# Kernel optimization log

Measured on AMD Instinct MI355X. Metric: run time of the kernel, lower is better.

The kernel has to match this reference:

```python
import jax, jax.numpy as jnp
import numpy as np

GAMMA = 0.9  # decay (init kwarg)


def setup_inputs() -> dict:
    key = jax.random.key(0)
    k0, k1, k2, k3 = jax.random.split(key, 4)
    B, T, D = 16, 2048, 256
    x = jax.random.normal(k0, (B, T, D), jnp.float32)
    scale = 1.0 / np.sqrt(D)
    Wq = jax.random.normal(k1, (D, D), jnp.float32) * scale
    Wk = jax.random.normal(k2, (D, D), jnp.float32) * scale
    Wv = jax.random.normal(k3, (D, D), jnp.float32) * scale
    return {"x": x, "Wq": Wq, "Wk": Wk, "Wv": Wv}


def reference(x, Wq, Wk, Wv):
    # x: [B, T, D]
    B, T, D = x.shape
    Q = x @ Wq  # [B, T, D]
    K = x @ Wk
    V = x @ Wv

    # Sequential retention recurrence over the [D, D] state:
    #   s[t] = gamma * s[t-1] + K[:, t, :]^T @ V[:, t, :]   (sums over batch, as in source)
    Kt = jnp.swapaxes(K, 0, 1)  # [T, B, D]
    Vt = jnp.swapaxes(V, 0, 1)  # [T, B, D]

    def step(s, kv):
        k_t, v_t = kv  # each [B, D]
        s = GAMMA * s + k_t.T @ v_t  # [D, D]
        return s, s.sum(-1)  # emit row-sum [D]

    # Loop runs t = 1 .. T-1 in the source (s starts at 0); s[0] := s[1].
    init = jnp.zeros((D, D), x.dtype)
    _, rows = jax.lax.scan(step, init, (Kt[1:], Vt[1:]))  # rows: [T-1, D]
    S = jnp.concatenate([rows[:1], rows], axis=0)  # [T, D]

    # Faithful to tf.reshape(S, [-1, seq_len]) then tf.transpose: a reshape-scramble,
    # NOT a plain transpose of S.
    S2 = S.reshape(D, T).T  # [T, D]
    return S2[None, :, :] * Q  # broadcast over batch -> [B, T, D]
```

## Files before the change

### kernel.cpp

```cpp
#include <hip/hip_runtime.h>
#include <math.h>


#define GAMMA_F 0.9f
#define T_LEN 2048
#define D_DIM 256
#define B_DIM 16

typedef __attribute__((ext_vector_type(8))) short bf16x8;
typedef __attribute__((ext_vector_type(16))) float f32x16;

__device__ inline ushort f2bf(float f) {
    union { float f; unsigned u; } v; v.f = f;
    unsigned r = (v.u + 0x7FFFu + ((v.u >> 16) & 1u)) >> 16;
    return (ushort)r;
}

__device__ __forceinline__ void gload_lds16(const void* g, void* l) {
    __builtin_amdgcn_global_load_lds(
        (const __attribute__((address_space(1))) unsigned int*)g,
        (__attribute__((address_space(3))) unsigned int*)l, 16, 0, 0);
}

__global__ __launch_bounds__(256) void k_prep(const float* __restrict__ Wq,
                                              const float* __restrict__ Wk,
                                              const float* __restrict__ Wv,
                                              ushort* __restrict__ WqT,
                                              ushort* __restrict__ WkT,
                                              float* __restrict__ wv_sum) {
    int bid = blockIdx.x;
    int tid = threadIdx.x;
    if (bid < 32) {
        __shared__ float tile[64][68];
        const float* W = (bid < 16) ? Wq : Wk;
        ushort* WT = (bid < 16) ? WqT : WkT;
        int b = bid & 15;
        int k0 = (b & 3) * 64;
        int n0 = (b >> 2) * 64;
        int r = tid >> 4;
        int c4 = (tid & 15) * 4;
#pragma unroll
        for (int i = 0; i < 4; ++i) {
            float4 v = *(const float4*)(W + (size_t)(k0 + r + 16 * i) * D_DIM + n0 + c4);
            *(float4*)&tile[r + 16 * i][c4] = v;
        }
        __syncthreads();
        int n = tid >> 2;
        int j0 = (tid & 3) * 16;
        ushort tmp[16];
#pragma unroll
        for (int i = 0; i < 16; ++i) tmp[i] = f2bf(tile[j0 + i][n]);
        ushort* dst = WT + (size_t)(n0 + n) * D_DIM + k0 + j0;
#pragma unroll
        for (int i = 0; i < 16; ++i) dst[i] = tmp[i];
    } else {
        int j = (bid - 32) * 64 + (tid >> 2);
        int q = tid & 3;
        const float4* row4 = (const float4*)(Wv + (size_t)j * D_DIM + q * 64);
        float s = 0.f;
#pragma unroll
        for (int i = 0; i < 16; ++i) {
            float4 v = row4[i];
            s += v.x + v.y + v.z + v.w;
        }
        s += __shfl_xor(s, 1, 64);
        s += __shfl_xor(s, 2, 64);
        if (q == 0) wv_sum[j] = s;
    }
}

__global__ __launch_bounds__(256) void k_y(const float* __restrict__ x,
                                           const float* __restrict__ wv_sum,
                                           ushort* __restrict__ ybf,
                                           ushort* __restrict__ xbf) {
    int t = blockIdx.x;
    int d = threadIdx.x;
    float wvd = wv_sum[d];
    float xr[B_DIM];
#pragma unroll
    for (int b = 0; b < B_DIM; ++b)
        xr[b] = x[((size_t)b * T_LEN + t) * D_DIM + d];

#pragma unroll
    for (int b = 0; b < B_DIM; ++b)
        xbf[((size_t)b * T_LEN + t) * D_DIM + d] = f2bf(xr[b]);

    __shared__ float red[B_DIM][4];
    int wave = d >> 6, lane = d & 63;
#pragma unroll
    for (int b = 0; b < B_DIM; ++b) {
        float p = xr[b] * wvd;
        for (int o = 32; o > 0; o >>= 1) p += __shfl_down(p, o, 64);
        if (lane == 0) red[b][wave] = p;
    }
    __syncthreads();
    float yv = 0.f;
#pragma unroll
    for (int b = 0; b < B_DIM; ++b) {
        float wb = red[b][0] + red[b][1] + red[b][2] + red[b][3];
        yv += wb * xr[b];
    }
    ybf[(size_t)t * D_DIM + d] = f2bf(yv);
}

__global__ __launch_bounds__(256) void k_gs(const ushort* __restrict__ ybf,
                                            const ushort* __restrict__ WkT,
                                            float* __restrict__ loc,
                                            float* __restrict__ carry) {
    __shared__ ushort As[32 * 64 * 8];
    __shared__ ushort Bs[32 * 64 * 8];
    float* Cs = (float*)As;
    int mt = blockIdx.x >> 2;
    int nt = blockIdx.x & 3;
    int tid = threadIdx.x, lane = tid & 63, w = tid >> 6;
    int wr = w >> 1, wc = w & 1, l31 = lane & 31, lh = lane >> 5;

#pragma unroll
    for (int i = 0; i < 8; ++i) {
        int slot = tid + 256 * i;
        int r = slot >> 5;
        int s2h = slot & 31;
        int rs = r ^ (s2h & 7);
        *(bf16x8*)&As[(s2h * 64 + rs) * 8] =
            *(const bf16x8*)&ybf[(size_t)(mt * 64 + r) * D_DIM + s2h * 8];
        *(bf16x8*)&Bs[(s2h * 64 + rs) * 8] =
            *(const bf16x8*)&WkT[(size_t)(nt * 64 + r) * D_DIM + s2h * 8];
    }
    __syncthreads();

    f32x16 acc;
#pragma unroll
    for (int e = 0; e < 16; ++e) acc[e] = 0.f;
#pragma unroll
    for (int s = 0; s < 16; ++s) {
        int s2h = s * 2 + lh;
        int ra = (wr * 32 + l31) ^ (s2h & 7);
        int rb = (wc * 32 + l31) ^ (s2h & 7);
        bf16x8 a = *(bf16x8*)&As[(s2h * 64 + ra) * 8];
        bf16x8 b = *(bf16x8*)&Bs[(s2h * 64 + rb) * 8];
        acc = __builtin_amdgcn_mfma_f32_32x32x16_bf16(a, b, acc, 0, 0, 0);
    }
    __syncthreads();

#pragma unroll
    for (int reg = 0; reg < 16; ++reg) {
        int rr = (reg & 3) + 8 * (reg >> 2) + 4 * lh;
        Cs[(wr * 32 + rr) * 64 + wc * 32 + l31] = acc[reg];
    }
    __syncthreads();

#pragma unroll
    for (int half = 0; half < 2; ++half) {
        int task = half * 256 + tid;
        int dl = task & 63;
        int cl = task >> 6;
        float a = 0.f;
#pragma unroll
        for (int j = 0; j < 8; ++j) {
            int tl = cl * 8 + j;
            int gt = mt * 64 + tl;
            float v = (gt == 0) ? 0.f : Cs[tl * 64 + dl];
            a = GAMMA_F * a + v;
            loc[(size_t)gt * D_DIM + nt * 64 + dl] = a;
        }
        carry[(size_t)(mt * 8 + cl) * D_DIM + nt * 64 + dl] = a;
    }
}

__global__ __launch_bounds__(256) void k_S2P(const float* __restrict__ loc,
                                             const float* __restrict__ carry,
                                             float* __restrict__ S2) {
    __shared__ float Ls[256][33];
    int o = blockIdx.x >> 3;
    int dseg = blockIdx.x & 7;
    int r = threadIdx.x;
    int dstart = dseg * 32;
    const float g8 = 0.43046721f;
    const float log2g = -0.15200309344504995f;
    float gp = exp2f((float)(o + 1) * log2g);

    float p = 0.f;
    int j0 = dstart - 32; if (j0 < 0) j0 = 0;
    for (int j = j0; j < dstart; ++j)
        p = p * g8 + carry[(size_t)j * D_DIM + r];

#pragma unroll
    for (int dd = 0; dd < 32; ++dd) {
        int d_ = dstart + dd;
        float Aval = loc[(size_t)(8 * d_ + o) * D_DIM + r] + gp * p;
        if (o == 0 && d_ == 0) Aval = loc[D_DIM + r];
        Ls[r][dd] = Aval;
        p = p * g8 + carry[(size_t)d_ * D_DIM + r];
    }
    __syncthreads();

    int rr = threadIdx.x >> 3;
    int cq = threadIdx.x & 7;
#pragma unroll
    for (int it = 0; it < 8; ++it) {
        int row = it * 32 + rr;
        float4 v;
        v.x = Ls[row][cq * 4 + 0];
        v.y = Ls[row][cq * 4 + 1];
        v.z = Ls[row][cq * 4 + 2];
        v.w = Ls[row][cq * 4 + 3];
        *(float4*)&S2[(size_t)((o << 8) + row) * D_DIM + dstart + cq * 4] = v;
    }
}

__global__ __launch_bounds__(256) void k_qgemm(const ushort* __restrict__ xbf,
                                               const ushort* __restrict__ WqT,
                                               const float* __restrict__ S2,
                                               float* __restrict__ out) {
    __shared__ ushort As[8 * 128 * 8];
    __shared__ ushort Bs[8 * 128 * 8];
    int bid = blockIdx.x;
    int mb = bid >> 1;
    int nb = bid & 1;
    int tid = threadIdx.x;
    int lane = tid & 63, w = tid >> 6;
    int wr = w >> 1, wc = w & 1;
    int l31 = lane & 31, lh = lane >> 5;

    f32x16 acc[2][2];
#pragma unroll
    for (int i = 0; i < 2; ++i)
#pragma unroll
        for (int j = 0; j < 2; ++j)
#pragma unroll
            for (int e = 0; e < 16; ++e) acc[i][j][e] = 0.f;

    const ushort* ab = xbf + (size_t)mb * 128 * D_DIM;
    const ushort* bb = WqT + (size_t)nb * 128 * D_DIM;

    for (int kb = 0; kb < 4; ++kb) {
#pragma unroll
        for (int i = 0; i < 4; ++i) {
            int slot = i * 256 + tid;
            int kk = slot >> 7;
            int row = slot & 127;
            int ldsbase = (i * 256 + w * 64) * 8;
            gload_lds16(ab + (size_t)row * D_DIM + kb * 64 + kk * 8, &As[ldsbase]);
            gload_lds16(bb + (size_t)row * D_DIM + kb * 64 + kk * 8, &Bs[ldsbase]);
        }
        __syncthreads();
#pragma unroll
        for (int s = 0; s < 4; ++s) {
            int c0 = (s * 2 + lh) * 128;
            bf16x8 a0 = *(bf16x8*)&As[(c0 + wr * 64 + l31) * 8];
            bf16x8 a1 = *(bf16x8*)&As[(c0 + wr * 64 + 32 + l31) * 8];
            bf16x8 b0 = *(bf16x8*)&Bs[(c0 + wc * 64 + l31) * 8];
            bf16x8 b1 = *(bf16x8*)&Bs[(c0 + wc * 64 + 32 + l31) * 8];
            acc[0][0] = __builtin_amdgcn_mfma_f32_32x32x16_bf16(a0, b0, acc[0][0], 0, 0, 0);
            acc[0][1] = __builtin_amdgcn_mfma_f32_32x32x16_bf16(a0, b1, acc[0][1], 0, 0, 0);
            acc[1][0] = __builtin_amdgcn_mfma_f32_32x32x16_bf16(a1, b0, acc[1][0], 0, 0, 0);
            acc[1][1] = __builtin_amdgcn_mfma_f32_32x32x16_bf16(a1, b1, acc[1][1], 0, 0, 0);
        }
        __syncthreads();
    }

    int t_base = (mb & 15) * 128;
    size_t row_base = (size_t)mb * 128;
#pragma unroll
    for (int mi = 0; mi < 2; ++mi) {
#pragma unroll
        for (int ni = 0; ni < 2; ++ni) {
            int gn = nb * 128 + wc * 64 + ni * 32 + l31;
#pragma unroll
            for (int reg = 0; reg < 16; ++reg) {
                int rr = (reg & 3) + 8 * (reg >> 2) + 4 * lh;
                int m = wr * 64 + mi * 32 + rr;
                float s2v = S2[(size_t)(t_base + m) * D_DIM + gn];
                out[(row_base + m) * D_DIM + gn] = acc[mi][ni][reg] * s2v;
            }
        }
    }
}

extern "C" void kernel_launch(void* const* d_in, const int* in_sizes, int n_in,
                              void* d_out, int out_size, void* d_ws, size_t ws_size,
                              hipStream_t stream) {
    const float* x  = (const float*)d_in[0];
    const float* Wq = (const float*)d_in[1];
    const float* Wk = (const float*)d_in[2];
    const float* Wv = (const float*)d_in[3];
    float* out = (float*)d_out;

    float* ws = (float*)d_ws;
    float* loc    = ws;
    float* S2     = loc + 524288;
    float* wv_sum = S2 + 524288;
    float* carry  = wv_sum + 256;
    ushort* WqT   = (ushort*)(carry + 65536);
    ushort* WkT   = WqT + 65536;
    ushort* ybf   = WkT + 65536;
    ushort* xbf   = ybf + 524288;

    k_prep<<<36, 256, 0, stream>>>(Wq, Wk, Wv, WqT, WkT, wv_sum);
    k_y<<<T_LEN, 256, 0, stream>>>(x, wv_sum, ybf, xbf);
    k_gs<<<128, 256, 0, stream>>>(ybf, WkT, loc, carry);
    k_S2P<<<64, 256, 0, stream>>>(loc, carry, S2);
    k_qgemm<<<(B_DIM * T_LEN / 128) * 2, 256, 0, stream>>>(xbf, WqT, S2, out);
}
```

Baseline: 130.8 us.

## Vectorize k_y per-wave rows and double-buffer k_qgemm LDS stages

```diff
diff --git a/kernel.cpp b/kernel.cpp
--- a/kernel.cpp
+++ b/kernel.cpp
@@ -73,34 +73,39 @@
                                            const float* __restrict__ wv_sum,
                                            ushort* __restrict__ ybf,
                                            ushort* __restrict__ xbf) {
-    int t = blockIdx.x;
-    int d = threadIdx.x;
-    float wvd = wv_sum[d];
-    float xr[B_DIM];
-#pragma unroll
-    for (int b = 0; b < B_DIM; ++b)
-        xr[b] = x[((size_t)b * T_LEN + t) * D_DIM + d];
-
-#pragma unroll
-    for (int b = 0; b < B_DIM; ++b)
-        xbf[((size_t)b * T_LEN + t) * D_DIM + d] = f2bf(xr[b]);
-
-    __shared__ float red[B_DIM][4];
-    int wave = d >> 6, lane = d & 63;
+    int tid = threadIdx.x;
+    int lane = tid & 63;
+    int t = blockIdx.x * 4 + (tid >> 6);
+    int d0 = lane * 4;
+    float4 wv4 = *(const float4*)(wv_sum + d0);
+
+    float4 xr[B_DIM];
+    float w[B_DIM];
 #pragma unroll
     for (int b = 0; b < B_DIM; ++b) {
-        float p = xr[b] * wvd;
-        for (int o = 32; o > 0; o >>= 1) p += __shfl_down(p, o, 64);
-        if (lane == 0) red[b][wave] = p;
-    }
-    __syncthreads();
-    float yv = 0.f;
+        xr[b] = *(const float4*)(x + ((size_t)b * T_LEN + t) * D_DIM + d0);
+        float p = xr[b].x * wv4.x + xr[b].y * wv4.y + xr[b].z * wv4.z + xr[b].w * wv4.w;
+#pragma unroll
+        for (int o = 32; o > 0; o >>= 1) p += __shfl_xor(p, o, 64);
+        w[b] = p;
+    }
+
+    float4 acc = make_float4(0.f, 0.f, 0.f, 0.f);
 #pragma unroll
     for (int b = 0; b < B_DIM; ++b) {
-        float wb = red[b][0] + red[b][1] + red[b][2] + red[b][3];
-        yv += wb * xr[b];
-    }
-    ybf[(size_t)t * D_DIM + d] = f2bf(yv);
+        acc.x += w[b] * xr[b].x;
+        acc.y += w[b] * xr[b].y;
+        acc.z += w[b] * xr[b].z;
+        acc.w += w[b] * xr[b].w;
+        ushort4 s;
+        s.x = f2bf(xr[b].x); s.y = f2bf(xr[b].y);
+        s.z = f2bf(xr[b].z); s.w = f2bf(xr[b].w);
+        *(ushort4*)&xbf[((size_t)b * T_LEN + t) * D_DIM + d0] = s;
+    }
+    ushort4 ys;
+    ys.x = f2bf(acc.x); ys.y = f2bf(acc.y);
+    ys.z = f2bf(acc.z); ys.w = f2bf(acc.w);
+    *(ushort4*)&ybf[(size_t)t * D_DIM + d0] = ys;
 }
 
 __global__ __launch_bounds__(256) void k_gs(const ushort* __restrict__ ybf,
@@ -212,8 +217,8 @@
                                                const ushort* __restrict__ WqT,
                                                const float* __restrict__ S2,
                                                float* __restrict__ out) {
-    __shared__ ushort As[8 * 128 * 8];
-    __shared__ ushort Bs[8 * 128 * 8];
+    __shared__ ushort As[2][8 * 128 * 8];
+    __shared__ ushort Bs[2][8 * 128 * 8];
     int bid = blockIdx.x;
     int mb = bid >> 1;
     int nb = bid & 1;
@@ -233,31 +238,43 @@
     const ushort* ab = xbf + (size_t)mb * 128 * D_DIM;
     const ushort* bb = WqT + (size_t)nb * 128 * D_DIM;
 
+#define STAGE(buf, kb)                                                        \
+    do {                                                                      \
+        _Pragma("unroll")                                                     \
+        for (int i = 0; i < 4; ++i) {                                         \
+            int slot = i * 256 + tid;             \
+            int kk = slot >> 7;                                               \
+            int row = slot & 127;                                             \
+            int ldsbase = (i * 256 + w * 64) * 8;      \
+            gload_lds16(ab + (size_t)row * D_DIM + (kb) * 64 + kk * 8,        \
+                        &As[buf][ldsbase]);                                   \
+            gload_lds16(bb + (size_t)row * D_DIM + (kb) * 64 + kk * 8,        \
+                        &Bs[buf][ldsbase]);                                   \
+        }                                                                     \
+    } while (0)
+
+    STAGE(0, 0);
+    __syncthreads();
+
+#pragma unroll
     for (int kb = 0; kb < 4; ++kb) {
-#pragma unroll
-        for (int i = 0; i < 4; ++i) {
-            int slot = i * 256 + tid;
-            int kk = slot >> 7;
-            int row = slot & 127;
-            int ldsbase = (i * 256 + w * 64) * 8;
-            gload_lds16(ab + (size_t)row * D_DIM + kb * 64 + kk * 8, &As[ldsbase]);
-            gload_lds16(bb + (size_t)row * D_DIM + kb * 64 + kk * 8, &Bs[ldsbase]);
-        }
-        __syncthreads();
+        int cur = kb & 1;
+        if (kb < 3) STAGE(cur ^ 1, kb + 1);
 #pragma unroll
         for (int s = 0; s < 4; ++s) {
             int c0 = (s * 2 + lh) * 128;
-            bf16x8 a0 = *(bf16x8*)&As[(c0 + wr * 64 + l31) * 8];
-            bf16x8 a1 = *(bf16x8*)&As[(c0 + wr * 64 + 32 + l31) * 8];
-            bf16x8 b0 = *(bf16x8*)&Bs[(c0 + wc * 64 + l31) * 8];
-            bf16x8 b1 = *(bf16x8*)&Bs[(c0 + wc * 64 + 32 + l31) * 8];
+            bf16x8 a0 = *(bf16x8*)&As[cur][(c0 + wr * 64 + l31) * 8];
+            bf16x8 a1 = *(bf16x8*)&As[cur][(c0 + wr * 64 + 32 + l31) * 8];
+            bf16x8 b0 = *(bf16x8*)&Bs[cur][(c0 + wc * 64 + l31) * 8];
+            bf16x8 b1 = *(bf16x8*)&Bs[cur][(c0 + wc * 64 + 32 + l31) * 8];
             acc[0][0] = __builtin_amdgcn_mfma_f32_32x32x16_bf16(a0, b0, acc[0][0], 0, 0, 0);
             acc[0][1] = __builtin_amdgcn_mfma_f32_32x32x16_bf16(a0, b1, acc[0][1], 0, 0, 0);
             acc[1][0] = __builtin_amdgcn_mfma_f32_32x32x16_bf16(a1, b0, acc[1][0], 0, 0, 0);
             acc[1][1] = __builtin_amdgcn_mfma_f32_32x32x16_bf16(a1, b1, acc[1][1], 0, 0, 0);
         }
-        __syncthreads();
-    }
+        if (kb < 3) __syncthreads();
+    }
+#undef STAGE
 
     int t_base = (mb & 15) * 128;
     size_t row_base = (size_t)mb * 128;
@@ -297,7 +314,7 @@
     ushort* xbf   = ybf + 524288;
 
     k_prep<<<36, 256, 0, stream>>>(Wq, Wk, Wv, WqT, WkT, wv_sum);
-    k_y<<<T_LEN, 256, 0, stream>>>(x, wv_sum, ybf, xbf);
+    k_y<<<T_LEN / 4, 256, 0, stream>>>(x, wv_sum, ybf, xbf);
     k_gs<<<128, 256, 0, stream>>>(ybf, WkT, loc, carry);
     k_S2P<<<64, 256, 0, stream>>>(loc, carry, S2);
     k_qgemm<<<(B_DIM * T_LEN / 128) * 2, 256, 0, stream>>>(xbf, WqT, S2, out);
```

Result: faster. 122.5 us (-6.4%).
